# Performance work log

Hardware: AMD Instinct MI355X
Metric: run time of the kernel (lower is better)

The kernel has to match this reference:

```python
import jax, jax.numpy as jnp
import numpy as np

N_NODES = 50000
N_EDGES = 800000
D = 128
SAME_W = 0.3
CROSS_W = 1.0


def setup_inputs() -> dict:
    key = jax.random.key(0)
    k1, k2, k3, k4, k5 = jax.random.split(key, 5)
    x = jax.random.normal(k1, (N_NODES, D), dtype=jnp.float32)
    edge_index = jax.random.randint(k2, (2, N_EDGES), 0, N_NODES, dtype=jnp.int64)
    edge_weight = jax.random.uniform(k3, (N_EDGES,), dtype=jnp.float32)
    Wr1 = jax.random.normal(k4, (D, D), dtype=jnp.float32) * (1.0 / np.sqrt(D))
    Wr2 = jax.random.normal(k5, (D, D), dtype=jnp.float32) * (1.0 / np.sqrt(D))
    return {"x": x, "edge_index": edge_index, "edge_weight": edge_weight,
            "Wr1": Wr1, "Wr2": Wr2, "cell_len": 20000}


def _node_types(idx, cell_len):
    # get_node_types: type 0 if idx <= cell_len, else 1 (note the <=, faithful to source)
    return (idx > cell_len).astype(jnp.int32)


def _conv_layer(x, src, dst, per_edge_w, Wr, n_nodes):
    # gather -> weight -> scatter-mean -> + root linear
    msg = x[src] * per_edge_w[:, None]                       # [E, D]
    agg = jax.ops.segment_sum(msg, dst, num_segments=n_nodes)  # [N, D]
    cnt = jax.ops.segment_sum(jnp.ones_like(per_edge_w), dst, num_segments=n_nodes)
    agg = agg / jnp.maximum(cnt, 1.0)[:, None]               # mean aggr (0 if no edges)
    return agg + x @ Wr.T                                     # lin_r, bias=False


def reference(x, edge_index, edge_weight, Wr1, Wr2, cell_len):
    src, dst = edge_index[0], edge_index[1]
    same = _node_types(src, cell_len) == _node_types(dst, cell_len)
    type_w = jnp.where(same, SAME_W, CROSS_W).astype(x.dtype)
    w = type_w * edge_weight                                  # [E]
    n_nodes = x.shape[0]
    h = _conv_layer(x, src, dst, w, Wr1, n_nodes)
    out = _conv_layer(h, src, dst, w, Wr2, n_nodes)
    return out
```

## Files before the change

### kernel.cpp

```cpp
#include <hip/hip_runtime.h>
#include <cstdint>
#include <cstddef>

#define D 128
#define SAME_W 0.3f
#define CROSS_W 1.0f
#define NSLICE 8
#define EPT 8
#define CAP 64
#define GEMM_BLOCKS 512

using bf16x8 = __attribute__((ext_vector_type(8))) __bf16;
using f32x4  = __attribute__((ext_vector_type(4))) float;

__device__ __forceinline__ unsigned bf16rne(float f) {
    unsigned u = __float_as_uint(f);
    return (u + 0x7FFFu + ((u >> 16) & 1u)) >> 16;
}

__global__ __launch_bounds__(256) void k_fill_capped(const int* __restrict__ src,
                                                     const int* __restrict__ dst,
                                                     const float* __restrict__ ew,
                                                     const int* __restrict__ cell_len,
                                                     int* __restrict__ cnt,
                                                     unsigned* __restrict__ meta,
                                                     int E, int sliceLen) {
    const int slice = blockIdx.x & (NSLICE - 1);
    const int lo = slice * sliceLen, hi = lo + sliceLen;
    const int base = (blockIdx.x >> 3) * (256 * EPT) + threadIdx.x;
    const int c = *cell_len;
    #pragma unroll
    for (int u = 0; u < EPT; ++u) {
        int e = base + u * 256;
        if (e < E) {
            int d = dst[e];
            if (d >= lo && d < hi) {
                int s = src[e];
                float wt = ew[e] * (((s > c) == (d > c)) ? SAME_W : CROSS_W);
                int pos = atomicAdd(&cnt[d], 1);
                if (pos < CAP)
                    meta[d * CAP + pos] = (unsigned)s | (bf16rne(wt) << 16);
            }
        }
    }
}

__global__ __launch_bounds__(256) void k_split4(const float4* __restrict__ in,
                                                uint2* __restrict__ oh,
                                                uint2* __restrict__ ol, int nvec) {
    int i = blockIdx.x * blockDim.x + threadIdx.x;
    if (i >= nvec) return;
    float4 v = in[i];
    unsigned h0 = bf16rne(v.x), h1 = bf16rne(v.y), h2 = bf16rne(v.z), h3 = bf16rne(v.w);
    uint2 rh;
    rh.x = h0 | (h1 << 16);
    rh.y = h2 | (h3 << 16);
    oh[i] = rh;
    float r0 = v.x - __uint_as_float(h0 << 16);
    float r1 = v.y - __uint_as_float(h1 << 16);
    float r2 = v.z - __uint_as_float(h2 << 16);
    float r3 = v.w - __uint_as_float(h3 << 16);
    uint2 rl;
    rl.x = bf16rne(r0) | (bf16rne(r1) << 16);
    rl.y = bf16rne(r2) | (bf16rne(r3) << 16);
    ol[i] = rl;
}

__global__ __launch_bounds__(256) void k_wcombine(const float* __restrict__ W1,
                                                  const float* __restrict__ W2,
                                                  unsigned* __restrict__ wsh,
                                                  unsigned* __restrict__ w12h,
                                                  unsigned* __restrict__ w12l) {
    int t = blockIdx.x * 256 + threadIdx.x;
    int j = t >> 6, kp = t & 63;
    int k0 = kp * 2;
    float d0 = 0.f, d1 = 0.f;
    #pragma unroll 4
    for (int m = 0; m < D; ++m) {
        float a = W2[j * D + m];
        d0 = fmaf(a, W1[m * D + k0], d0);
        d1 = fmaf(a, W1[m * D + k0 + 1], d1);
    }
    float s0 = W1[j * D + k0] + W2[j * D + k0];
    float s1 = W1[j * D + k0 + 1] + W2[j * D + k0 + 1];
    wsh[j * 64 + kp] = bf16rne(s0) | (bf16rne(s1) << 16);
    unsigned h0 = bf16rne(d0), h1 = bf16rne(d1);
    w12h[j * 64 + kp] = h0 | (h1 << 16);
    float r0 = d0 - __uint_as_float(h0 << 16);
    float r1 = d1 - __uint_as_float(h1 << 16);
    w12l[j * 64 + kp] = bf16rne(r0) | (bf16rne(r1) << 16);
}

__global__ __launch_bounds__(256) void k_agg_cap(const unsigned* __restrict__ xin,
                                                 const uint4* __restrict__ meta4,
                                                 const int* __restrict__ cnt,
                                                 unsigned* __restrict__ outp, int N) {
    int gid = blockIdx.x * blockDim.x + threadIdx.x;
    int node = gid >> 6;
    int lane = gid & 63;
    if (node >= N) return;
    const int cn0 = cnt[node];
    const int cn = min(cn0, CAP);
    const uint4* mrow = meta4 + (size_t)node * (CAP / 4);
    float ax0 = 0.f, ay0 = 0.f, ax1 = 0.f, ay1 = 0.f;
    int i = 0;
    #pragma unroll 1
    for (; i + 16 <= cn; i += 16) {
        uint4 mq[4];
        #pragma unroll
        for (int u = 0; u < 4; ++u) mq[u] = mrow[(i >> 2) + u];
        unsigned v[16];
        #pragma unroll
        for (int u = 0; u < 16; ++u) {
            unsigned m = ((const unsigned*)mq)[u];
            v[u] = xin[(size_t)(m & 0xFFFFu) * 64 + lane];
        }
        #pragma unroll
        for (int u = 0; u < 16; ++u) {
            unsigned m = ((const unsigned*)mq)[u];
            float wt = __uint_as_float(m & 0xFFFF0000u);
            float vx = __uint_as_float(v[u] << 16);
            float vy = __uint_as_float(v[u] & 0xFFFF0000u);
            if (u & 1) { ax1 = fmaf(vx, wt, ax1); ay1 = fmaf(vy, wt, ay1); }
            else       { ax0 = fmaf(vx, wt, ax0); ay0 = fmaf(vy, wt, ay0); }
        }
    }
    #pragma unroll 1
    for (; i + 4 <= cn; i += 4) {
        uint4 mq = mrow[i >> 2];
        unsigned v[4];
        #pragma unroll
        for (int u = 0; u < 4; ++u)
            v[u] = xin[(size_t)(((const unsigned*)&mq)[u] & 0xFFFFu) * 64 + lane];
        #pragma unroll
        for (int u = 0; u < 4; ++u) {
            unsigned m = ((const unsigned*)&mq)[u];
            float wt = __uint_as_float(m & 0xFFFF0000u);
            float vx = __uint_as_float(v[u] << 16);
            float vy = __uint_as_float(v[u] & 0xFFFF0000u);
            if (u & 1) { ax1 = fmaf(vx, wt, ax1); ay1 = fmaf(vy, wt, ay1); }
            else       { ax0 = fmaf(vx, wt, ax0); ay0 = fmaf(vy, wt, ay0); }
        }
    }
    for (; i < cn; ++i) {
        unsigned m = ((const unsigned*)mrow)[i];
        float wt = __uint_as_float(m & 0xFFFF0000u);
        unsigned v = xin[(size_t)(m & 0xFFFFu) * 64 + lane];
        ax0 = fmaf(__uint_as_float(v << 16), wt, ax0);
        ay0 = fmaf(__uint_as_float(v & 0xFFFF0000u), wt, ay0);
    }
    const float scale = 1.0f / (float)max(cn0, 1);
    const float rx = (ax0 + ax1) * scale, ry = (ay0 + ay1) * scale;
    outp[(size_t)node * 64 + lane] = bf16rne(rx) | (bf16rne(ry) << 16);
}

__global__ __launch_bounds__(256, 2) void k_gemm2(
    const uint4* __restrict__ xh4, const uint4* __restrict__ xl4,
    const uint4* __restrict__ a1h4,
    const uint4* __restrict__ w12h4, const uint4* __restrict__ w12l4,
    const uint4* __restrict__ wsh4,
    const unsigned* __restrict__ a2b,
    float* __restrict__ fout, int N, int nTiles)
{
    const int t = threadIdx.x;
    const int wave = t >> 6, lane = t & 63;
    const int j0 = wave * 32;
    const int lr = lane & 15;
    const int q  = lane >> 4;

    union FU { uint4 u; bf16x8 v; };

    FU wA[2][4], wB[2][4], wC[2][4];
    #pragma unroll
    for (int jt = 0; jt < 2; ++jt) {
        const int brow = (j0 + jt * 16 + lr) * 16 + q;
        #pragma unroll
        for (int ks = 0; ks < 4; ++ks) {
            wA[jt][ks].u = w12h4[brow + ks * 4];
            wB[jt][ks].u = w12l4[brow + ks * 4];
            wC[jt][ks].u = wsh4[brow + ks * 4];
        }
    }

#define LOAD_TILE(BX, BL, BA, BC, TILE) do {                                   \
    int row_ = (TILE) * 16 + lr; if (row_ > N - 1) row_ = N - 1;               \
    const int ar_ = row_ * 16 + q;                                             \
    _Pragma("unroll")                                                          \
    for (int ks = 0; ks < 4; ++ks) {                                           \
        BX[ks].u = xh4[ar_ + ks * 4];                                          \
        BL[ks].u = xl4[ar_ + ks * 4];                                          \
        BA[ks].u = a1h4[ar_ + ks * 4];                                         \
    }                                                                          \
    _Pragma("unroll")                                                          \
    for (int jt = 0; jt < 2; ++jt)                                             \
        _Pragma("unroll")                                                      \
        for (int r = 0; r < 4; ++r) {                                          \
            int rr_ = (TILE) * 16 + q * 4 + r; if (rr_ > N - 1) rr_ = N - 1;   \
            BC[jt * 4 + r] = a2b[(size_t)rr_ * 64 + ((j0 + jt * 16 + lr) >> 1)]; \
        }                                                                      \
} while (0)

#define COMPUTE_STORE(BX, BL, BA, BC, TILE) do {                               \
    f32x4 c_[2];                                                               \
    c_[0] = (f32x4){0.f, 0.f, 0.f, 0.f};                                       \
    c_[1] = (f32x4){0.f, 0.f, 0.f, 0.f};                                       \
    _Pragma("unroll")                                                          \
    for (int jt = 0; jt < 2; ++jt)                                             \
        _Pragma("unroll")                                                      \
        for (int ks = 0; ks < 4; ++ks) {                                       \
            c_[jt] = __builtin_amdgcn_mfma_f32_16x16x32_bf16(BX[ks].v, wA[jt][ks].v, c_[jt], 0, 0, 0); \
            c_[jt] = __builtin_amdgcn_mfma_f32_16x16x32_bf16(BL[ks].v, wA[jt][ks].v, c_[jt], 0, 0, 0); \
            c_[jt] = __builtin_amdgcn_mfma_f32_16x16x32_bf16(BX[ks].v, wB[jt][ks].v, c_[jt], 0, 0, 0); \
            c_[jt] = __builtin_amdgcn_mfma_f32_16x16x32_bf16(BA[ks].v, wC[jt][ks].v, c_[jt], 0, 0, 0); \
        }                                                                      \
    _Pragma("unroll")                                                          \
    for (int jt = 0; jt < 2; ++jt)                                             \
        _Pragma("unroll")                                                      \
        for (int r = 0; r < 4; ++r) {                                          \
            int rr_ = (TILE) * 16 + q * 4 + r;                                 \
            if (rr_ < N) {                                                     \
                unsigned w_ = BC[jt * 4 + r];                                  \
                float ci_ = __uint_as_float((lr & 1) ? (w_ & 0xFFFF0000u) : (w_ << 16)); \
                fout[(size_t)rr_ * D + j0 + jt * 16 + lr] = c_[jt][r] + ci_;   \
            }                                                                  \
        }                                                                      \
} while (0)

    FU Axh[4], Axl[4], Aa1[4]; unsigned Aci[8];
    FU Bxh[4], Bxl[4], Ba1[4]; unsigned Bci[8];

    int tile = blockIdx.x;
    const int step = gridDim.x;
    if (tile >= nTiles) return;
    LOAD_TILE(Axh, Axl, Aa1, Aci, tile);
    while (true) {
        int tn = tile + step;
        if (tn < nTiles) LOAD_TILE(Bxh, Bxl, Ba1, Bci, tn);
        COMPUTE_STORE(Axh, Axl, Aa1, Aci, tile);
        tile = tn;
        if (tile >= nTiles) break;
        tn = tile + step;
        if (tn < nTiles) LOAD_TILE(Axh, Axl, Aa1, Aci, tn);
        COMPUTE_STORE(Bxh, Bxl, Ba1, Bci, tile);
        tile = tn;
        if (tile >= nTiles) break;
    }
#undef LOAD_TILE
#undef COMPUTE_STORE
}

extern "C" void kernel_launch(void* const* d_in, const int* in_sizes, int n_in,
                              void* d_out, int out_size, void* d_ws, size_t ws_size,
                              hipStream_t stream) {
    const float* x        = (const float*)d_in[0];
    const int*   ei       = (const int*)d_in[1];
    const float* ew       = (const float*)d_in[2];
    const float* Wr1      = (const float*)d_in[3];
    const float* Wr2      = (const float*)d_in[4];
    const int*   cell_len = (const int*)d_in[5];

    const int N = in_sizes[0] / D;
    const int E = in_sizes[1] / 2;
    const int* src = ei;
    const int* dst = ei + E;

    char* ws = (char*)d_ws;
    size_t off = 0;
    unsigned* meta = (unsigned*)(ws + off); off += (size_t)4 * CAP * N;
    int*      cnt  = (int*)     (ws + off); off += (size_t)4 * N;
    off = (off + 255) & ~(size_t)255;
    unsigned* xh   = (unsigned*)(ws + off); off += (size_t)2 * N * D;
    unsigned* xl   = (unsigned*)(ws + off); off += (size_t)2 * N * D;
    unsigned* a1h  = (unsigned*)(ws + off); off += (size_t)2 * N * D;
    unsigned* a2b  = (unsigned*)(ws + off); off += (size_t)2 * N * D;
    unsigned* wsh  = (unsigned*)(ws + off); off += (size_t)2 * D * D;
    unsigned* w12h = (unsigned*)(ws + off); off += (size_t)2 * D * D;
    unsigned* w12l = (unsigned*)(ws + off); off += (size_t)2 * D * D;
    if (ws_size < off) return;
    float* out = (float*)d_out;

    hipMemsetAsync(cnt, 0, (size_t)4 * N, stream);

    const int sliceLen = (N + NSLICE - 1) / NSLICE;
    const int edgeBlocks = ((E + 256 * EPT - 1) / (256 * EPT)) * NSLICE;
    const int aggBlocks = (N + 3) / 4;
    const int nTiles = (N + 15) / 16;
    const int xvec = N * D / 4;

    k_fill_capped<<<edgeBlocks, 256, 0, stream>>>(src, dst, ew, cell_len,
                                                  cnt, meta, E, sliceLen);
    k_split4<<<(xvec + 255) / 256, 256, 0, stream>>>((const float4*)x,
                                                     (uint2*)xh, (uint2*)xl, xvec);
    k_wcombine<<<32, 256, 0, stream>>>(Wr1, Wr2, wsh, w12h, w12l);

    k_agg_cap<<<aggBlocks, 256, 0, stream>>>(xh, (const uint4*)meta, cnt, a1h, N);
    k_agg_cap<<<aggBlocks, 256, 0, stream>>>(a1h, (const uint4*)meta, cnt, a2b, N);

    k_gemm2<<<GEMM_BLOCKS, 256, 0, stream>>>((const uint4*)xh, (const uint4*)xl,
                                             (const uint4*)a1h,
                                             (const uint4*)w12h, (const uint4*)w12l,
                                             (const uint4*)wsh, a2b, out, N, nTiles);
}
```

Baseline: 232.5 us.

## Gather node features in FP8 for aggregation and merge preprocessing kernels

Adds an FP8 (e4m3) copy of x and of the first-layer aggregate. Both scatter-mean passes now gather 2-byte FP8 pairs instead of 4-byte bf16 pairs, which halves the random-gather traffic that dominates aggregation. The edge fill, x split and weight-combine kernels are merged into one launch with block-range dispatch, and the edge loads become non-temporal. The cost is a large precision loss in the aggregated features, which risks failing accuracy tolerance.

```diff
diff --git a/kernel.cpp b/kernel.cpp
--- a/kernel.cpp
+++ b/kernel.cpp
@@ -18,83 +18,83 @@
     return (u + 0x7FFFu + ((u >> 16) & 1u)) >> 16;
 }
 
-__global__ __launch_bounds__(256) void k_fill_capped(const int* __restrict__ src,
-                                                     const int* __restrict__ dst,
-                                                     const float* __restrict__ ew,
-                                                     const int* __restrict__ cell_len,
-                                                     int* __restrict__ cnt,
-                                                     unsigned* __restrict__ meta,
-                                                     int E, int sliceLen) {
-    const int slice = blockIdx.x & (NSLICE - 1);
-    const int lo = slice * sliceLen, hi = lo + sliceLen;
-    const int base = (blockIdx.x >> 3) * (256 * EPT) + threadIdx.x;
-    const int c = *cell_len;
-    #pragma unroll
-    for (int u = 0; u < EPT; ++u) {
-        int e = base + u * 256;
-        if (e < E) {
-            int d = dst[e];
-            if (d >= lo && d < hi) {
-                int s = src[e];
-                float wt = ew[e] * (((s > c) == (d > c)) ? SAME_W : CROSS_W);
-                int pos = atomicAdd(&cnt[d], 1);
-                if (pos < CAP)
-                    meta[d * CAP + pos] = (unsigned)s | (bf16rne(wt) << 16);
+__global__ __launch_bounds__(256) void k_pre(
+    const int* __restrict__ src, const int* __restrict__ dst,
+    const float* __restrict__ ew, const int* __restrict__ cell_len,
+    int* __restrict__ cnt, unsigned* __restrict__ meta, int E, int sliceLen,
+    int nFill,
+    const float4* __restrict__ x4, uint2* __restrict__ xh2,
+    uint2* __restrict__ xl2, unsigned* __restrict__ xq, int nvec, int nSplit,
+    const float* __restrict__ W1, const float* __restrict__ W2,
+    unsigned* __restrict__ wsh, unsigned* __restrict__ w12h,
+    unsigned* __restrict__ w12l)
+{
+    const int b = blockIdx.x;
+    if (b < nFill) {
+        const int slice = b & (NSLICE - 1);
+        const int lo = slice * sliceLen, hi = lo + sliceLen;
+        const int base = (b >> 3) * (256 * EPT) + threadIdx.x;
+        const int c = *cell_len;
+        #pragma unroll
+        for (int u = 0; u < EPT; ++u) {
+            int e = base + u * 256;
+            if (e < E) {
+                int d = __builtin_nontemporal_load(&dst[e]);
+                if (d >= lo && d < hi) {
+                    int s = __builtin_nontemporal_load(&src[e]);
+                    float w = __builtin_nontemporal_load(&ew[e]);
+                    float wt = w * (((s > c) == (d > c)) ? SAME_W : CROSS_W);
+                    int pos = atomicAdd(&cnt[d], 1);
+                    if (pos < CAP)
+                        meta[d * CAP + pos] = (unsigned)s | (bf16rne(wt) << 16);
+                }
             }
         }
-    }
-}
-
-__global__ __launch_bounds__(256) void k_split4(const float4* __restrict__ in,
-                                                uint2* __restrict__ oh,
-                                                uint2* __restrict__ ol, int nvec) {
-    int i = blockIdx.x * blockDim.x + threadIdx.x;
-    if (i >= nvec) return;
-    float4 v = in[i];
-    unsigned h0 = bf16rne(v.x), h1 = bf16rne(v.y), h2 = bf16rne(v.z), h3 = bf16rne(v.w);
-    uint2 rh;
-    rh.x = h0 | (h1 << 16);
-    rh.y = h2 | (h3 << 16);
-    oh[i] = rh;
-    float r0 = v.x - __uint_as_float(h0 << 16);
-    float r1 = v.y - __uint_as_float(h1 << 16);
-    float r2 = v.z - __uint_as_float(h2 << 16);
-    float r3 = v.w - __uint_as_float(h3 << 16);
-    uint2 rl;
-    rl.x = bf16rne(r0) | (bf16rne(r1) << 16);
-    rl.y = bf16rne(r2) | (bf16rne(r3) << 16);
-    ol[i] = rl;
-}
-
-__global__ __launch_bounds__(256) void k_wcombine(const float* __restrict__ W1,
-                                                  const float* __restrict__ W2,
-                                                  unsigned* __restrict__ wsh,
-                                                  unsigned* __restrict__ w12h,
-                                                  unsigned* __restrict__ w12l) {
-    int t = blockIdx.x * 256 + threadIdx.x;
-    int j = t >> 6, kp = t & 63;
-    int k0 = kp * 2;
-    float d0 = 0.f, d1 = 0.f;
-    #pragma unroll 4
-    for (int m = 0; m < D; ++m) {
-        float a = W2[j * D + m];
-        d0 = fmaf(a, W1[m * D + k0], d0);
-        d1 = fmaf(a, W1[m * D + k0 + 1], d1);
-    }
-    float s0 = W1[j * D + k0] + W2[j * D + k0];
-    float s1 = W1[j * D + k0 + 1] + W2[j * D + k0 + 1];
-    wsh[j * 64 + kp] = bf16rne(s0) | (bf16rne(s1) << 16);
-    unsigned h0 = bf16rne(d0), h1 = bf16rne(d1);
-    w12h[j * 64 + kp] = h0 | (h1 << 16);
-    float r0 = d0 - __uint_as_float(h0 << 16);
-    float r1 = d1 - __uint_as_float(h1 << 16);
-    w12l[j * 64 + kp] = bf16rne(r0) | (bf16rne(r1) << 16);
-}
-
-__global__ __launch_bounds__(256) void k_agg_cap(const unsigned* __restrict__ xin,
+    } else if (b < nFill + nSplit) {
+        int i = (b - nFill) * 256 + threadIdx.x;
+        if (i >= nvec) return;
+        float4 v = x4[i];
+        unsigned h0 = bf16rne(v.x), h1 = bf16rne(v.y),
+                 h2 = bf16rne(v.z), h3 = bf16rne(v.w);
+        xh2[i] = make_uint2(h0 | (h1 << 16), h2 | (h3 << 16));
+        float r0 = v.x - __uint_as_float(h0 << 16);
+        float r1 = v.y - __uint_as_float(h1 << 16);
+        float r2 = v.z - __uint_as_float(h2 << 16);
+        float r3 = v.w - __uint_as_float(h3 << 16);
+        xl2[i] = make_uint2(bf16rne(r0) | (bf16rne(r1) << 16),
+                            bf16rne(r2) | (bf16rne(r3) << 16));
+        int q = __builtin_amdgcn_cvt_pk_fp8_f32(v.x, v.y, 0, false);
+        q = __builtin_amdgcn_cvt_pk_fp8_f32(v.z, v.w, q, true);
+        xq[i] = (unsigned)q;
+    } else {
+        int t = (b - nFill - nSplit) * 256 + threadIdx.x;
+        int j = t >> 6, kp = t & 63;
+        int k0 = kp * 2;
+        float d0 = 0.f, d1 = 0.f;
+        #pragma unroll 4
+        for (int m = 0; m < D; ++m) {
+            float a = W2[j * D + m];
+            d0 = fmaf(a, W1[m * D + k0], d0);
+            d1 = fmaf(a, W1[m * D + k0 + 1], d1);
+        }
+        float s0 = W1[j * D + k0] + W2[j * D + k0];
+        float s1 = W1[j * D + k0 + 1] + W2[j * D + k0 + 1];
+        wsh[j * 64 + kp] = bf16rne(s0) | (bf16rne(s1) << 16);
+        unsigned h0 = bf16rne(d0), h1 = bf16rne(d1);
+        w12h[j * 64 + kp] = h0 | (h1 << 16);
+        float r0 = d0 - __uint_as_float(h0 << 16);
+        float r1 = d1 - __uint_as_float(h1 << 16);
+        w12l[j * 64 + kp] = bf16rne(r0) | (bf16rne(r1) << 16);
+    }
+}
+
+template <bool EMIT_FP8>
+__global__ __launch_bounds__(256) void k_agg_fp8(const unsigned short* __restrict__ xq,
                                                  const uint4* __restrict__ meta4,
                                                  const int* __restrict__ cnt,
-                                                 unsigned* __restrict__ outp, int N) {
+                                                 unsigned* __restrict__ outb,
+                                                 unsigned short* __restrict__ outq,
+                                                 int N) {
     int gid = blockIdx.x * blockDim.x + threadIdx.x;
     int node = gid >> 6;
     int lane = gid & 63;
@@ -109,18 +109,18 @@
         uint4 mq[4];
         #pragma unroll
         for (int u = 0; u < 4; ++u) mq[u] = mrow[(i >> 2) + u];
-        unsigned v[16];
+        unsigned short v[16];
         #pragma unroll
         for (int u = 0; u < 16; ++u) {
             unsigned m = ((const unsigned*)mq)[u];
-            v[u] = xin[(size_t)(m & 0xFFFFu) * 64 + lane];
+            v[u] = xq[(size_t)(m & 0xFFFFu) * 64 + lane];
         }
         #pragma unroll
         for (int u = 0; u < 16; ++u) {
             unsigned m = ((const unsigned*)mq)[u];
             float wt = __uint_as_float(m & 0xFFFF0000u);
-            float vx = __uint_as_float(v[u] << 16);
-            float vy = __uint_as_float(v[u] & 0xFFFF0000u);
+            float vx = __builtin_amdgcn_cvt_f32_fp8((unsigned)v[u], 0);
+            float vy = __builtin_amdgcn_cvt_f32_fp8((unsigned)v[u], 1);
             if (u & 1) { ax1 = fmaf(vx, wt, ax1); ay1 = fmaf(vy, wt, ay1); }
             else       { ax0 = fmaf(vx, wt, ax0); ay0 = fmaf(vy, wt, ay0); }
         }
@@ -128,16 +128,16 @@
     #pragma unroll 1
     for (; i + 4 <= cn; i += 4) {
         uint4 mq = mrow[i >> 2];
-        unsigned v[4];
+        unsigned short v[4];
         #pragma unroll
         for (int u = 0; u < 4; ++u)
-            v[u] = xin[(size_t)(((const unsigned*)&mq)[u] & 0xFFFFu) * 64 + lane];
+            v[u] = xq[(size_t)(((const unsigned*)&mq)[u] & 0xFFFFu) * 64 + lane];
         #pragma unroll
         for (int u = 0; u < 4; ++u) {
             unsigned m = ((const unsigned*)&mq)[u];
             float wt = __uint_as_float(m & 0xFFFF0000u);
-            float vx = __uint_as_float(v[u] << 16);
-            float vy = __uint_as_float(v[u] & 0xFFFF0000u);
+            float vx = __builtin_amdgcn_cvt_f32_fp8((unsigned)v[u], 0);
+            float vy = __builtin_amdgcn_cvt_f32_fp8((unsigned)v[u], 1);
             if (u & 1) { ax1 = fmaf(vx, wt, ax1); ay1 = fmaf(vy, wt, ay1); }
             else       { ax0 = fmaf(vx, wt, ax0); ay0 = fmaf(vy, wt, ay0); }
         }
@@ -145,13 +145,17 @@
     for (; i < cn; ++i) {
         unsigned m = ((const unsigned*)mrow)[i];
         float wt = __uint_as_float(m & 0xFFFF0000u);
-        unsigned v = xin[(size_t)(m & 0xFFFFu) * 64 + lane];
-        ax0 = fmaf(__uint_as_float(v << 16), wt, ax0);
-        ay0 = fmaf(__uint_as_float(v & 0xFFFF0000u), wt, ay0);
+        unsigned short v = xq[(size_t)(m & 0xFFFFu) * 64 + lane];
+        ax0 = fmaf(__builtin_amdgcn_cvt_f32_fp8((unsigned)v, 0), wt, ax0);
+        ay0 = fmaf(__builtin_amdgcn_cvt_f32_fp8((unsigned)v, 1), wt, ay0);
     }
     const float scale = 1.0f / (float)max(cn0, 1);
     const float rx = (ax0 + ax1) * scale, ry = (ay0 + ay1) * scale;
-    outp[(size_t)node * 64 + lane] = bf16rne(rx) | (bf16rne(ry) << 16);
+    outb[(size_t)node * 64 + lane] = bf16rne(rx) | (bf16rne(ry) << 16);
+    if (EMIT_FP8) {
+        int q = __builtin_amdgcn_cvt_pk_fp8_f32(rx, ry, 0, false);
+        outq[(size_t)node * 64 + lane] = (unsigned short)(q & 0xFFFF);
+    }
 }
 
 __global__ __launch_bounds__(256, 2) void k_gemm2(
@@ -273,6 +277,8 @@
     unsigned* xl   = (unsigned*)(ws + off); off += (size_t)2 * N * D;
     unsigned* a1h  = (unsigned*)(ws + off); off += (size_t)2 * N * D;
     unsigned* a2b  = (unsigned*)(ws + off); off += (size_t)2 * N * D;
+    unsigned* xq   = (unsigned*)(ws + off); off += (size_t)1 * N * D;
+    unsigned* a1q  = (unsigned*)(ws + off); off += (size_t)1 * N * D;
     unsigned* wsh  = (unsigned*)(ws + off); off += (size_t)2 * D * D;
     unsigned* w12h = (unsigned*)(ws + off); off += (size_t)2 * D * D;
     unsigned* w12l = (unsigned*)(ws + off); off += (size_t)2 * D * D;
@@ -282,19 +288,24 @@
     hipMemsetAsync(cnt, 0, (size_t)4 * N, stream);
 
     const int sliceLen = (N + NSLICE - 1) / NSLICE;
-    const int edgeBlocks = ((E + 256 * EPT - 1) / (256 * EPT)) * NSLICE;
+    const int nFill  = ((E + 256 * EPT - 1) / (256 * EPT)) * NSLICE;
+    const int xvec   = N * D / 4;
+    const int nSplit = (xvec + 255) / 256;
+    const int nW     = (D * 64 + 255) / 256;
     const int aggBlocks = (N + 3) / 4;
     const int nTiles = (N + 15) / 16;
-    const int xvec = N * D / 4;
-
-    k_fill_capped<<<edgeBlocks, 256, 0, stream>>>(src, dst, ew, cell_len,
-                                                  cnt, meta, E, sliceLen);
-    k_split4<<<(xvec + 255) / 256, 256, 0, stream>>>((const float4*)x,
-                                                     (uint2*)xh, (uint2*)xl, xvec);
-    k_wcombine<<<32, 256, 0, stream>>>(Wr1, Wr2, wsh, w12h, w12l);
-
-    k_agg_cap<<<aggBlocks, 256, 0, stream>>>(xh, (const uint4*)meta, cnt, a1h, N);
-    k_agg_cap<<<aggBlocks, 256, 0, stream>>>(a1h, (const uint4*)meta, cnt, a2b, N);
+
+    k_pre<<<nFill + nSplit + nW, 256, 0, stream>>>(
+        src, dst, ew, cell_len, cnt, meta, E, sliceLen, nFill,
+        (const float4*)x, (uint2*)xh, (uint2*)xl, xq, xvec, nSplit,
+        Wr1, Wr2, wsh, w12h, w12l);
+
+    k_agg_fp8<true ><<<aggBlocks, 256, 0, stream>>>(
+        (const unsigned short*)xq, (const uint4*)meta, cnt,
+        a1h, (unsigned short*)a1q, N);
+    k_agg_fp8<false><<<aggBlocks, 256, 0, stream>>>(
+        (const unsigned short*)a1q, (const uint4*)meta, cnt,
+        a2b, nullptr, N);
 
     k_gemm2<<<GEMM_BLOCKS, 256, 0, stream>>>((const uint4*)xh, (const uint4*)xl,
                                              (const uint4*)a1h,
```

Result: faster. 225.4 us (-3.0%).
